# Kernel optimization log

Hardware: AMD Instinct MI355X
Metric: run time of the kernel (lower is better)

The kernel has to match this reference:

```python
import jax, jax.numpy as jnp
import numpy as np

N, D, H = 4096, 2048, 16
HD = D // H
NEG = -1e9


def setup_inputs() -> dict:
    key = jax.random.key(0)
    ks = jax.random.split(key, 9)
    s = 1.0 / np.sqrt(D)
    x = jax.random.normal(ks[0], (N, D), dtype=jnp.float32)
    # additive causal mask: 0 on/below diag, -1e9 above
    causal = jnp.where(jnp.tril(jnp.ones((N, N), dtype=bool)), 0.0, NEG).astype(jnp.float32)
    return {
        "x": x,
        "attn_mask": causal,
        "Wq": jax.random.uniform(ks[1], (D, D), jnp.float32, -s, s),
        "bq": jax.random.uniform(ks[2], (D,), jnp.float32, -s, s),
        "Wk": jax.random.uniform(ks[3], (D, D), jnp.float32, -s, s),
        "bk": jax.random.uniform(ks[4], (D,), jnp.float32, -s, s),
        "Wv": jax.random.uniform(ks[5], (D, D), jnp.float32, -s, s),
        "bv": jax.random.uniform(ks[6], (D,), jnp.float32, -s, s),
        "Wo": jax.random.uniform(ks[7], (D, D), jnp.float32, -s, s),
        "bo": jax.random.uniform(ks[8], (D,), jnp.float32, -s, s),
    }


def reference(x, attn_mask, Wq, bq, Wk, bk, Wv, bv, Wo, bo):
    scale = 1.0 / np.sqrt(HD)

    def heads(t):  # (N, D) -> (H, N, HD)
        return jnp.transpose(t.reshape(N, H, HD), (1, 0, 2))

    q = heads(x @ Wq.T + bq)
    k = heads(x @ Wk.T + bk)
    v = heads(x @ Wv.T + bv)
    attn = jnp.einsum('hnd,hmd->hnm', q, k) * scale + attn_mask
    attn = jax.nn.softmax(attn, axis=-1)
    out = jnp.einsum('hnm,hmd->hnd', attn, v)
    out = jnp.transpose(out, (1, 0, 2)).reshape(N, D)
    return out @ Wo.T + bo
```

## Files before the change

### kernel.cpp

```cpp
#include <hip/hip_runtime.h>
#include <stdint.h>


#define N_TOK   4096
#define D_MODEL 2048
#define N_HEADS 16
#define HD_DIM  128

typedef __attribute__((ext_vector_type(8))) short short8;
typedef __attribute__((ext_vector_type(4))) float f32x4;
typedef __attribute__((ext_vector_type(16))) float f32x16;

static __device__ __forceinline__ unsigned short f2bf(float f) {
    union { float f; uint32_t u; } v; v.f = f;
    uint32_t r = v.u + 0x7fffu + ((v.u >> 16) & 1u);
    return (unsigned short)(r >> 16);
}

static __device__ __forceinline__ float exp2fast(float x) {
    float r; asm("v_exp_f32 %0, %1" : "=v"(r) : "v"(x)); return r;
}

static __device__ __forceinline__ unsigned cvtpk_bf16(float lo, float hi) {
    unsigned r; asm("v_cvt_pk_bf16_f32 %0, %1, %2" : "=v"(r) : "v"(lo), "v"(hi));
    return r;
}

static __device__ __forceinline__ void gload_lds16(const void* g, void* l) {
    __builtin_amdgcn_global_load_lds(
        (const __attribute__((address_space(1))) void*)g,
        (__attribute__((address_space(3))) void*)l,
        16, 0, 0);
}

#define XG  2097152
#define WG  1048576
__global__ void cvt_all(const float* __restrict__ x,
                        const float* __restrict__ Wq, const float* __restrict__ Wk,
                        const float* __restrict__ Wv, const float* __restrict__ Wo,
                        unsigned short* __restrict__ xb,
                        unsigned short* __restrict__ Wqb, unsigned short* __restrict__ Wkb,
                        unsigned short* __restrict__ Wvb, unsigned short* __restrict__ Wob) {
    int i = blockIdx.x * blockDim.x + threadIdx.x;
    int stride = gridDim.x * blockDim.x;
    for (; i < XG + 4 * WG; i += stride) {
        const float* s; unsigned short* d; int j;
        if (i < XG) { s = x; d = xb; j = i; }
        else {
            int t = i - XG; int wsel = t >> 20; j = t & (WG - 1);
            if (wsel == 0)      { s = Wq; d = Wqb; }
            else if (wsel == 1) { s = Wk; d = Wkb; }
            else if (wsel == 2) { s = Wv; d = Wvb; }
            else                { s = Wo; d = Wob; }
        }
        float4 f = reinterpret_cast<const float4*>(s)[j];
        ushort4 o;
        o.x = f2bf(f.x); o.y = f2bf(f.y); o.z = f2bf(f.z); o.w = f2bf(f.w);
        reinterpret_cast<ushort4*>(d)[j] = o;
    }
}

#define BM 128
#define BN 128
#define BK 64

template<int OUT_BF16>
static __device__ __forceinline__ void gemm_body(
    const unsigned short* __restrict__ A, int lda,
    const unsigned short* __restrict__ B, int ldb,
    void* __restrict__ Cv, int ldc,
    const float* __restrict__ bias, int bias_row,
    int K, int row0, int col0,
    unsigned short* As, unsigned short* Bs)
{
    const int tid = threadIdx.x;
    const int w = tid >> 6, l = tid & 63;
    const int wr = w >> 1, wc = w & 1;
    const int l15 = l & 15, l4 = l >> 4;

    f32x4 acc[4][4] = {};

    const int srow = tid >> 3;
    const int ske  = (((tid & 7) * 16) ^ ((srow & 7) << 4)) >> 1;

    for (int kt = 0; kt < K; kt += BK) {
#pragma unroll
        for (int c = 0; c < 4; ++c)
            gload_lds16(A + (size_t)(row0 + c * 32 + srow) * lda + kt + ske,
                        As + c * 2048 + w * 512);
#pragma unroll
        for (int c = 0; c < 4; ++c)
            gload_lds16(B + (size_t)(col0 + c * 32 + srow) * ldb + kt + ske,
                        Bs + c * 2048 + w * 512);
        __syncthreads();
#pragma unroll
        for (int s = 0; s < 2; ++s) {
            short8 af[4], bf[4];
#pragma unroll
            for (int mt = 0; mt < 4; ++mt) {
                int r = wr * 64 + mt * 16 + l15;
                int kb = (s * 64 + l4 * 16) ^ ((r & 7) << 4);
                af[mt] = *reinterpret_cast<const short8*>((const char*)As + r * 128 + kb);
            }
#pragma unroll
            for (int nt = 0; nt < 4; ++nt) {
                int r = wc * 64 + nt * 16 + l15;
                int kb = (s * 64 + l4 * 16) ^ ((r & 7) << 4);
                bf[nt] = *reinterpret_cast<const short8*>((const char*)Bs + r * 128 + kb);
            }
#pragma unroll
            for (int mt = 0; mt < 4; ++mt)
#pragma unroll
                for (int nt = 0; nt < 4; ++nt)
                    acc[mt][nt] = __builtin_amdgcn_mfma_f32_16x16x32_bf16(
                        af[mt], bf[nt], acc[mt][nt], 0, 0, 0);
        }
        __syncthreads();
    }

#pragma unroll
    for (int mt = 0; mt < 4; ++mt)
#pragma unroll
        for (int nt = 0; nt < 4; ++nt) {
            int col = col0 + wc * 64 + nt * 16 + l15;
#pragma unroll
            for (int r_ = 0; r_ < 4; ++r_) {
                int row = row0 + wr * 64 + mt * 16 + l4 * 4 + r_;
                float v = acc[mt][nt][r_] + (bias_row ? bias[row] : bias[col]);
                if (OUT_BF16)
                    ((unsigned short*)Cv)[(size_t)row * ldc + col] = f2bf(v);
                else
                    ((float*)Cv)[(size_t)row * ldc + col] = v;
            }
        }
}

__global__ __launch_bounds__(256) void gemm_qkv(
    const unsigned short* __restrict__ xb,
    const unsigned short* __restrict__ Wqb,
    const unsigned short* __restrict__ Wkb,
    const unsigned short* __restrict__ Wvb,
    const float* __restrict__ bq, const float* __restrict__ bk,
    const float* __restrict__ bv,
    unsigned short* __restrict__ Qb, unsigned short* __restrict__ Kb,
    unsigned short* __restrict__ Vtb)
{
    __shared__ __align__(16) unsigned short As[BM * BK];
    __shared__ __align__(16) unsigned short Bs[BN * BK];

    int b = blockIdx.x;
    b = (b & 7) * 192 + (b >> 3);

    const unsigned short *A, *B;
    unsigned short* C;
    const float* bias;
    int row0, col0, ldc, brow;
    if (b < 1024) {
        row0 = (b >> 5) * BM;
        int col = (b & 31) * BN;
        A = xb;
        if (col < 2048) { B = Wqb; C = Qb; bias = bq; col0 = col; }
        else            { B = Wkb; C = Kb; bias = bk; col0 = col - 2048; }
        ldc = 2048; brow = 0;
    } else {
        int v = b - 1024;
        row0 = (v >> 5) * BM;
        col0 = (v & 31) * BN;
        A = Wvb; B = xb; C = Vtb; bias = bv; ldc = 4096; brow = 1;
    }
    gemm_body<1>(A, D_MODEL, B, D_MODEL, C, ldc, bias, brow,
                 D_MODEL, row0, col0, As, Bs);
}

__global__ __launch_bounds__(256) void gemm_proj(
    const unsigned short* __restrict__ Ob,
    const unsigned short* __restrict__ Wob,
    float* __restrict__ out, const float* __restrict__ bo)
{
    __shared__ __align__(16) unsigned short As[BM * BK];
    __shared__ __align__(16) unsigned short Bs[BN * BK];
    const int nwg = gridDim.x * gridDim.y;
    int bid = blockIdx.y * gridDim.x + blockIdx.x;
    bid = (bid & 7) * (nwg >> 3) + (bid >> 3);
    const int row0 = (bid / gridDim.x) * BM;
    const int col0 = (bid % gridDim.x) * BN;
    gemm_body<0>(Ob, D_MODEL, Wob, D_MODEL, out, D_MODEL, bo, 0,
                 D_MODEL, row0, col0, As, Bs);
}

__global__ __launch_bounds__(128) void attn_kernel(
    const unsigned short* __restrict__ Qb,
    const unsigned short* __restrict__ Kb,
    const unsigned short* __restrict__ Vtb,
    unsigned short* __restrict__ Ob)
{
    __shared__ __align__(16) unsigned short Ks[64 * 128];
    const int tid = threadIdx.x;
    const int w = tid >> 6, l = tid & 63;
    const int l31 = l & 31, hi = l >> 5;

    int bid = blockIdx.y * gridDim.x + blockIdx.x;
    bid = (bid & 7) * 128 + (bid >> 3);
    const int h = bid >> 6;
    const int qi = 63 - (bid & 63);
    const int q0 = qi * 64;
    const int qw = q0 + w * 32;
    const float scale2 = 0.12753139f;

    short8 qreg[8];
#pragma unroll
    for (int s = 0; s < 8; ++s)
        qreg[s] = *reinterpret_cast<const short8*>(
            Qb + (size_t)(qw + l31) * D_MODEL + h * HD_DIM + s * 16 + hi * 8);

    float m = -1e30f, lsum = 0.f;
    f32x16 oacc[4] = {};

    const int nkt = qi + 1;

    const int krow_c = tid >> 4;
    const int kslot  = tid & 15;

    for (int kt = 0; kt < nkt; ++kt) {
        const int kv0 = kt * 64;
        if (kt) __syncthreads();
#pragma unroll
        for (int c = 0; c < 8; ++c) {
            int row = c * 8 + krow_c;
            gload_lds16(Kb + (size_t)(kv0 + row) * D_MODEL + h * HD_DIM
                           + (kslot ^ (row & 15)) * 8,
                        Ks + c * 1024 + w * 512);
        }
        __syncthreads();

        f32x16 sacc[2] = {};
#pragma unroll
        for (int s = 0; s < 8; ++s)
#pragma unroll
            for (int a = 0; a < 2; ++a) {
                int row = a * 32 + l31;
                int slot = (2 * s + hi) ^ (row & 15);
                short8 kf = *reinterpret_cast<const short8*>(
                    (const char*)Ks + row * 256 + slot * 16);
                sacc[a] = __builtin_amdgcn_mfma_f32_32x32x16_bf16(
                    kf, qreg[s], sacc[a], 0, 0, 0);
            }

        float tmax = -1e30f;
        if (kv0 + 64 > qw) {
#pragma unroll
            for (int a = 0; a < 2; ++a)
#pragma unroll
                for (int r = 0; r < 16; ++r) {
                    int kvl = a * 32 + (r & 3) + 8 * (r >> 2) + 4 * hi;
                    float x = sacc[a][r];
                    x = (kv0 + kvl > qw + l31) ? -1e30f : x;
                    sacc[a][r] = x;
                    tmax = fmaxf(tmax, x);
                }
        } else {
#pragma unroll
            for (int a = 0; a < 2; ++a)
#pragma unroll
                for (int r = 0; r < 16; ++r) tmax = fmaxf(tmax, sacc[a][r]);
        }
        tmax = fmaxf(tmax, __shfl_xor(tmax, 32));

        if (__any(tmax > m + 90.2f)) {
            float mnew = fmaxf(m, tmax);
            float alpha = exp2fast((m - mnew) * scale2);
            m = mnew;
            lsum *= alpha;
#pragma unroll
            for (int r = 0; r < 16; ++r) {
                float ar = __shfl(alpha, (r & 3) + 8 * (r >> 2) + 4 * hi, 32);
#pragma unroll
                for (int cb = 0; cb < 4; ++cb) oacc[cb][r] *= ar;
            }
        }

        const float mc = m * scale2;
        float rsum = 0.f;
#pragma unroll
        for (int a = 0; a < 2; ++a)
#pragma unroll
            for (int r = 0; r < 16; ++r) {
                float p = exp2fast(fmaf(sacc[a][r], scale2, -mc));
                sacc[a][r] = p;
                rsum += p;
            }
        rsum += __shfl_xor(rsum, 32);
        lsum += rsum;

#pragma unroll
        for (int st = 0; st < 4; ++st) {
            const int sl = st & 1, a = st >> 1;
            unsigned A0 = cvtpk_bf16(sacc[a][8 * sl + 0], sacc[a][8 * sl + 1]);
            unsigned A1 = cvtpk_bf16(sacc[a][8 * sl + 2], sacc[a][8 * sl + 3]);
            unsigned B0 = cvtpk_bf16(sacc[a][8 * sl + 4], sacc[a][8 * sl + 5]);
            unsigned B1 = cvtpk_bf16(sacc[a][8 * sl + 6], sacc[a][8 * sl + 7]);
            asm volatile("v_permlane32_swap_b32 %0, %1" : "+v"(A0), "+v"(B0));
            asm volatile("v_permlane32_swap_b32 %0, %1" : "+v"(A1), "+v"(B1));
            union { unsigned u[4]; short8 s8; } pu;
            pu.u[0] = A0; pu.u[1] = A1; pu.u[2] = B0; pu.u[3] = B1;
#pragma unroll
            for (int cb = 0; cb < 4; ++cb) {
                short8 vf = *reinterpret_cast<const short8*>(
                    Vtb + (size_t)(h * HD_DIM + cb * 32 + l31) * N_TOK
                        + kv0 + (2 * st + hi) * 8);
                oacc[cb] = __builtin_amdgcn_mfma_f32_32x32x16_bf16(
                    pu.s8, vf, oacc[cb], 0, 0, 0);
            }
        }
    }

    float linv = 1.f / lsum;
#pragma unroll
    for (int r = 0; r < 16; ++r) {
        int jr = (r & 3) + 8 * (r >> 2) + 4 * hi;
        float lr = __shfl(linv, jr, 32);
        int qrow = qw + jr;
#pragma unroll
        for (int cb = 0; cb < 4; ++cb)
            Ob[(size_t)qrow * D_MODEL + h * HD_DIM + cb * 32 + l31] =
                f2bf(oacc[cb][r] * lr);
    }
}

extern "C" void kernel_launch(void* const* d_in, const int* in_sizes, int n_in,
                              void* d_out, int out_size, void* d_ws, size_t ws_size,
                              hipStream_t stream) {
    const float* x  = (const float*)d_in[0];
    const float* Wq = (const float*)d_in[2];
    const float* bq = (const float*)d_in[3];
    const float* Wk = (const float*)d_in[4];
    const float* bk = (const float*)d_in[5];
    const float* Wv = (const float*)d_in[6];
    const float* bv = (const float*)d_in[7];
    const float* Wo = (const float*)d_in[8];
    const float* bo = (const float*)d_in[9];

    char* ws = (char*)d_ws;
    unsigned short* xb  = (unsigned short*)(ws);
    unsigned short* Wqb = (unsigned short*)(ws + ((size_t)16 << 20));
    unsigned short* Wkb = (unsigned short*)(ws + ((size_t)24 << 20));
    unsigned short* Wvb = (unsigned short*)(ws + ((size_t)32 << 20));
    unsigned short* Wob = (unsigned short*)(ws + ((size_t)40 << 20));
    unsigned short* Qb  = (unsigned short*)(ws + ((size_t)48 << 20));
    unsigned short* Kb  = (unsigned short*)(ws + ((size_t)64 << 20));
    unsigned short* Vtb = (unsigned short*)(ws + ((size_t)80 << 20));
    unsigned short* Ob  = (unsigned short*)(ws + ((size_t)96 << 20));

    cvt_all<<<2048, 256, 0, stream>>>(x, Wq, Wk, Wv, Wo,
                                      xb, Wqb, Wkb, Wvb, Wob);

    gemm_qkv<<<1536, 256, 0, stream>>>(xb, Wqb, Wkb, Wvb, bq, bk, bv,
                                       Qb, Kb, Vtb);

    attn_kernel<<<dim3(64, N_HEADS), 128, 0, stream>>>(Qb, Kb, Vtb, Ob);

    gemm_proj<<<dim3(D_MODEL / BN, N_TOK / BM), 256, 0, stream>>>(
        Ob, Wob, (float*)d_out, bo);
}
```

Measured before the change: 519.2 us.

## Pair causal query tiles per block and double-buffer K/V tiles in LDS

Each attention block now processes two query tiles (qi and 63-qi) so every block does the same amount of causal work, halving the grid to 512 blocks. K and V tiles are staged into double-buffered LDS with async global-to-LDS loads, so the next tile is prefetched while the current one is computed. V fragments are now read from swizzled LDS instead of straight from global memory. This raises LDS use to 64KB per block, which may lower occupancy, and fewer blocks may leave some CUs underused.

```diff
diff --git a/kernel.cpp b/kernel.cpp
--- a/kernel.cpp
+++ b/kernel.cpp
@@ -194,136 +194,159 @@
     const unsigned short* __restrict__ Vtb,
     unsigned short* __restrict__ Ob)
 {
-    __shared__ __align__(16) unsigned short Ks[64 * 128];
+    __shared__ __align__(16) unsigned short Ks[2][64 * 128];
+    __shared__ __align__(16) unsigned short Vs[2][128 * 64];
     const int tid = threadIdx.x;
     const int w = tid >> 6, l = tid & 63;
     const int l31 = l & 31, hi = l >> 5;
 
-    int bid = blockIdx.y * gridDim.x + blockIdx.x;
-    bid = (bid & 7) * 128 + (bid >> 3);
-    const int h = bid >> 6;
-    const int qi = 63 - (bid & 63);
-    const int q0 = qi * 64;
-    const int qw = q0 + w * 32;
+    int bid = blockIdx.x;
+    bid = (bid & 7) * 64 + (bid >> 3);
+    const int h = bid >> 5;
+    const int p = bid & 31;
     const float scale2 = 0.12753139f;
-
-    short8 qreg[8];
-#pragma unroll
-    for (int s = 0; s < 8; ++s)
-        qreg[s] = *reinterpret_cast<const short8*>(
-            Qb + (size_t)(qw + l31) * D_MODEL + h * HD_DIM + s * 16 + hi * 8);
-
-    float m = -1e30f, lsum = 0.f;
-    f32x16 oacc[4] = {};
-
-    const int nkt = qi + 1;
 
     const int krow_c = tid >> 4;
     const int kslot  = tid & 15;
-
-    for (int kt = 0; kt < nkt; ++kt) {
-        const int kv0 = kt * 64;
-        if (kt) __syncthreads();
+    const int vrow_c = tid >> 3;
+    const int vslot  = tid & 7;
+
+    auto stage = [&](int kt, int buf) {
+        const int kv0s = kt * 64;
 #pragma unroll
         for (int c = 0; c < 8; ++c) {
             int row = c * 8 + krow_c;
-            gload_lds16(Kb + (size_t)(kv0 + row) * D_MODEL + h * HD_DIM
+            gload_lds16(Kb + (size_t)(kv0s + row) * D_MODEL + h * HD_DIM
                            + (kslot ^ (row & 15)) * 8,
-                        Ks + c * 1024 + w * 512);
-        }
+                        Ks[buf] + c * 1024 + w * 512);
+        }
+#pragma unroll
+        for (int c = 0; c < 8; ++c) {
+            int row = c * 16 + vrow_c;
+            gload_lds16(Vtb + (size_t)(h * HD_DIM + row) * N_TOK + kv0s
+                            + (vslot ^ (row & 7)) * 8,
+                        Vs[buf] + c * 1024 + w * 512);
+        }
+    };
+
+#pragma unroll 1
+    for (int half = 0; half < 2; ++half) {
+        const int qi = half ? p : 63 - p;
+        const int qw = qi * 64 + w * 32;
+        const int nkt = qi + 1;
+
+        short8 qreg[8];
+#pragma unroll
+        for (int s = 0; s < 8; ++s)
+            qreg[s] = *reinterpret_cast<const short8*>(
+                Qb + (size_t)(qw + l31) * D_MODEL + h * HD_DIM + s * 16 + hi * 8);
+
+        float m = -1e30f, lsum = 0.f;
+        f32x16 oacc[4] = {};
+
+        stage(0, 0);
         __syncthreads();
 
-        f32x16 sacc[2] = {};
-#pragma unroll
-        for (int s = 0; s < 8; ++s)
-#pragma unroll
-            for (int a = 0; a < 2; ++a) {
-                int row = a * 32 + l31;
-                int slot = (2 * s + hi) ^ (row & 15);
-                short8 kf = *reinterpret_cast<const short8*>(
-                    (const char*)Ks + row * 256 + slot * 16);
-                sacc[a] = __builtin_amdgcn_mfma_f32_32x32x16_bf16(
-                    kf, qreg[s], sacc[a], 0, 0, 0);
-            }
-
-        float tmax = -1e30f;
-        if (kv0 + 64 > qw) {
+        int cur = 0;
+        for (int kt = 0; kt < nkt; ++kt) {
+            if (kt + 1 < nkt) stage(kt + 1, cur ^ 1);
+            const int kv0 = kt * 64;
+
+            f32x16 sacc[2] = {};
+#pragma unroll
+            for (int s = 0; s < 8; ++s)
+#pragma unroll
+                for (int a = 0; a < 2; ++a) {
+                    int row = a * 32 + l31;
+                    int slot = (2 * s + hi) ^ (row & 15);
+                    short8 kf = *reinterpret_cast<const short8*>(
+                        (const char*)Ks[cur] + row * 256 + slot * 16);
+                    sacc[a] = __builtin_amdgcn_mfma_f32_32x32x16_bf16(
+                        kf, qreg[s], sacc[a], 0, 0, 0);
+                }
+
+            float tmax = -1e30f;
+            if (kv0 + 64 > qw) {
+#pragma unroll
+                for (int a = 0; a < 2; ++a)
+#pragma unroll
+                    for (int r = 0; r < 16; ++r) {
+                        int kvl = a * 32 + (r & 3) + 8 * (r >> 2) + 4 * hi;
+                        float x = sacc[a][r];
+                        x = (kv0 + kvl > qw + l31) ? -1e30f : x;
+                        sacc[a][r] = x;
+                        tmax = fmaxf(tmax, x);
+                    }
+            } else {
+#pragma unroll
+                for (int a = 0; a < 2; ++a)
+#pragma unroll
+                    for (int r = 0; r < 16; ++r) tmax = fmaxf(tmax, sacc[a][r]);
+            }
+            tmax = fmaxf(tmax, __shfl_xor(tmax, 32));
+
+            if (__any(tmax > m + 90.2f)) {
+                float mnew = fmaxf(m, tmax);
+                float alpha = exp2fast((m - mnew) * scale2);
+                m = mnew;
+                lsum *= alpha;
+#pragma unroll
+                for (int r = 0; r < 16; ++r) {
+                    float ar = __shfl(alpha, (r & 3) + 8 * (r >> 2) + 4 * hi, 32);
+#pragma unroll
+                    for (int cb = 0; cb < 4; ++cb) oacc[cb][r] *= ar;
+                }
+            }
+
+            const float mc = m * scale2;
+            float rsum = 0.f;
 #pragma unroll
             for (int a = 0; a < 2; ++a)
 #pragma unroll
                 for (int r = 0; r < 16; ++r) {
-                    int kvl = a * 32 + (r & 3) + 8 * (r >> 2) + 4 * hi;
-                    float x = sacc[a][r];
-                    x = (kv0 + kvl > qw + l31) ? -1e30f : x;
-                    sacc[a][r] = x;
-                    tmax = fmaxf(tmax, x);
+                    float pe = exp2fast(fmaf(sacc[a][r], scale2, -mc));
+                    sacc[a][r] = pe;
+                    rsum += pe;
                 }
-        } else {
-#pragma unroll
-            for (int a = 0; a < 2; ++a)
-#pragma unroll
-                for (int r = 0; r < 16; ++r) tmax = fmaxf(tmax, sacc[a][r]);
-        }
-        tmax = fmaxf(tmax, __shfl_xor(tmax, 32));
-
-        if (__any(tmax > m + 90.2f)) {
-            float mnew = fmaxf(m, tmax);
-            float alpha = exp2fast((m - mnew) * scale2);
-            m = mnew;
-            lsum *= alpha;
-#pragma unroll
-            for (int r = 0; r < 16; ++r) {
-                float ar = __shfl(alpha, (r & 3) + 8 * (r >> 2) + 4 * hi, 32);
-#pragma unroll
-                for (int cb = 0; cb < 4; ++cb) oacc[cb][r] *= ar;
-            }
-        }
-
-        const float mc = m * scale2;
-        float rsum = 0.f;
-#pragma unroll
-        for (int a = 0; a < 2; ++a)
-#pragma unroll
-            for (int r = 0; r < 16; ++r) {
-                float p = exp2fast(fmaf(sacc[a][r], scale2, -mc));
-                sacc[a][r] = p;
-                rsum += p;
-            }
-        rsum += __shfl_xor(rsum, 32);
-        lsum += rsum;
-
-#pragma unroll
-        for (int st = 0; st < 4; ++st) {
-            const int sl = st & 1, a = st >> 1;
-            unsigned A0 = cvtpk_bf16(sacc[a][8 * sl + 0], sacc[a][8 * sl + 1]);
-            unsigned A1 = cvtpk_bf16(sacc[a][8 * sl + 2], sacc[a][8 * sl + 3]);
-            unsigned B0 = cvtpk_bf16(sacc[a][8 * sl + 4], sacc[a][8 * sl + 5]);
-            unsigned B1 = cvtpk_bf16(sacc[a][8 * sl + 6], sacc[a][8 * sl + 7]);
-            asm volatile("v_permlane32_swap_b32 %0, %1" : "+v"(A0), "+v"(B0));
-            asm volatile("v_permlane32_swap_b32 %0, %1" : "+v"(A1), "+v"(B1));
-            union { unsigned u[4]; short8 s8; } pu;
-            pu.u[0] = A0; pu.u[1] = A1; pu.u[2] = B0; pu.u[3] = B1;
-#pragma unroll
-            for (int cb = 0; cb < 4; ++cb) {
-                short8 vf = *reinterpret_cast<const short8*>(
-                    Vtb + (size_t)(h * HD_DIM + cb * 32 + l31) * N_TOK
-                        + kv0 + (2 * st + hi) * 8);
-                oacc[cb] = __builtin_amdgcn_mfma_f32_32x32x16_bf16(
-                    pu.s8, vf, oacc[cb], 0, 0, 0);
-            }
-        }
-    }
-
-    float linv = 1.f / lsum;
-#pragma unroll
-    for (int r = 0; r < 16; ++r) {
-        int jr = (r & 3) + 8 * (r >> 2) + 4 * hi;
-        float lr = __shfl(linv, jr, 32);
-        int qrow = qw + jr;
-#pragma unroll
-        for (int cb = 0; cb < 4; ++cb)
-            Ob[(size_t)qrow * D_MODEL + h * HD_DIM + cb * 32 + l31] =
-                f2bf(oacc[cb][r] * lr);
+            rsum += __shfl_xor(rsum, 32);
+            lsum += rsum;
+
+#pragma unroll
+            for (int st = 0; st < 4; ++st) {
+                const int sl = st & 1, a = st >> 1;
+                unsigned A0 = cvtpk_bf16(sacc[a][8 * sl + 0], sacc[a][8 * sl + 1]);
+                unsigned A1 = cvtpk_bf16(sacc[a][8 * sl + 2], sacc[a][8 * sl + 3]);
+                unsigned B0 = cvtpk_bf16(sacc[a][8 * sl + 4], sacc[a][8 * sl + 5]);
+                unsigned B1 = cvtpk_bf16(sacc[a][8 * sl + 6], sacc[a][8 * sl + 7]);
+                asm volatile("v_permlane32_swap_b32 %0, %1" : "+v"(A0), "+v"(B0));
+                asm volatile("v_permlane32_swap_b32 %0, %1" : "+v"(A1), "+v"(B1));
+                union { unsigned u[4]; short8 s8; } pu;
+                pu.u[0] = A0; pu.u[1] = A1; pu.u[2] = B0; pu.u[3] = B1;
+#pragma unroll
+                for (int cb = 0; cb < 4; ++cb) {
+                    int row = cb * 32 + l31;
+                    int slot = (2 * st + hi) ^ (row & 7);
+                    short8 vf = *reinterpret_cast<const short8*>(
+                        (const char*)Vs[cur] + row * 128 + slot * 16);
+                    oacc[cb] = __builtin_amdgcn_mfma_f32_32x32x16_bf16(
+                        pu.s8, vf, oacc[cb], 0, 0, 0);
+                }
+            }
+            __syncthreads();
+            cur ^= 1;
+        }
+
+        float linv = 1.f / lsum;
+#pragma unroll
+        for (int r = 0; r < 16; ++r) {
+            int jr = (r & 3) + 8 * (r >> 2) + 4 * hi;
+            float lr = __shfl(linv, jr, 32);
+            int qrow = qw + jr;
+#pragma unroll
+            for (int cb = 0; cb < 4; ++cb)
+                Ob[(size_t)qrow * D_MODEL + h * HD_DIM + cb * 32 + l31] =
+                    f2bf(oacc[cb][r] * lr);
+        }
     }
 }
 
@@ -357,7 +380,7 @@
     gemm_qkv<<<1536, 256, 0, stream>>>(xb, Wqb, Wkb, Wvb, bq, bk, bv,
                                        Qb, Kb, Vtb);
 
-    attn_kernel<<<dim3(64, N_HEADS), 128, 0, stream>>>(Qb, Kb, Vtb, Ob);
+    attn_kernel<<<512, 128, 0, stream>>>(Qb, Kb, Vtb, Ob);
 
     gemm_proj<<<dim3(D_MODEL / BN, N_TOK / BM), 256, 0, stream>>>(
         Ob, Wob, (float*)d_out, bo);
```

After: 473.4 us. 1.1x faster.
